# Performance work log

Hardware: AMD Instinct MI355X
Metric: run time of the kernel (lower is better)

The kernel has to match this reference:

```python
import jax, jax.numpy as jnp
import numpy as np

DIM = 512
NUM_HEADS = 16
WS = 8  # window_size
N = WS * WS
B = 1024


def get_relative_index(h, w):
    coords_h = np.arange(h)[:, None].repeat(w, axis=1)
    coords_w = np.arange(w)[None, :].repeat(h, axis=0)
    coords = np.stack([coords_h, coords_w], axis=-1).reshape(-1, 2)  # [N,2]
    rel = coords[:, None, :] - coords[None, :, :]
    rel = rel + np.array([h - 1, w - 1])
    rel[:, :, 0] *= 2 * w - 1
    return rel.sum(-1).astype(np.int32)  # [N,N]


def setup_inputs() -> dict:
    key = jax.random.key(0)
    ks = jax.random.split(key, 6)
    table_size = (2 * WS - 1) * (2 * WS - 1)  # 225
    return {
        "x": jax.random.normal(ks[0], (B, N, DIM), dtype=jnp.float32),
        "qkv_weight": jax.random.normal(ks[1], (3 * DIM, DIM), dtype=jnp.float32) * 0.02,
        "qkv_bias": jax.random.normal(ks[2], (3 * DIM,), dtype=jnp.float32) * 0.02,
        "proj_weight": jax.random.normal(ks[3], (DIM, DIM), dtype=jnp.float32) * 0.02,
        "proj_bias": jax.random.normal(ks[4], (DIM,), dtype=jnp.float32) * 0.02,
        "relative_table": jax.random.normal(ks[5], (table_size, 2 * NUM_HEADS), dtype=jnp.float32) * 0.02,
        "relative_index": jnp.asarray(get_relative_index(WS, WS)),
    }


def reference(x, qkv_weight, qkv_bias, proj_weight, proj_bias, relative_table, relative_index):
    B_, n, C = x.shape
    H = NUM_HEADS
    hd = C // H
    scale = hd ** -0.5
    # qkv projection: [B,N,3C] -> [3,B,H,N,hd]
    qkv = (x @ qkv_weight.T + qkv_bias).reshape(B_, n, 3, H, hd).transpose(2, 0, 3, 1, 4)
    q, k, v = qkv[0], qkv[1], qkv[2]
    attn = jnp.einsum("bhnd,bhmd->bhnm", q * scale, k)  # [B,H,N,N]
    # learned relative-position bias + post-softmax scale
    params = relative_table[relative_index.reshape(-1)].reshape(n, n, 2 * H)
    params = params.transpose(2, 0, 1)  # [2H,N,N]
    rel_bias, rel_scale = params[:H], params[H:]
    attn = jax.nn.softmax(attn + rel_bias[None], axis=-1)
    attn = attn * rel_scale[None]
    out = jnp.einsum("bhnm,bhmd->bhnd", attn, v)
    out = out.transpose(0, 2, 1, 3).reshape(B_, n, C)
    return out @ proj_weight.T + proj_bias
```

## Files before the change

### kernel.cpp

```cpp
#include <hip/hip_runtime.h>

typedef unsigned short u16;
typedef unsigned int   u32;
typedef __attribute__((ext_vector_type(8))) short bf16x8;
typedef __attribute__((ext_vector_type(4))) float f32x4;

#define SCALE 0.17677669529663687f

__device__ __forceinline__ u16 f2bf(float f){
  u32 x = __float_as_uint(f);
  x += 0x7fffu + ((x >> 16) & 1u);
  return (u16)(x >> 16);
}
__device__ __forceinline__ float bf2f(u16 u){
  return __uint_as_float(((u32)u) << 16);
}


__global__ void prep_kernel(const float* __restrict__ qkvw, const float* __restrict__ projw,
                            const float* __restrict__ table, const int* __restrict__ relidx,
                            u16* __restrict__ qkvw_b, u16* __restrict__ projw_b,
                            u16* __restrict__ biasT, u16* __restrict__ scaleT){
  int i = blockIdx.x * 256 + threadIdx.x;
  if (i < 786432) {
    qkvw_b[i] = f2bf(qkvw[i]);
  } else if (i < 1048576) {
    int j = i - 786432; projw_b[j] = f2bf(projw[j]);
  } else if (i < 1114112) {
    int j = i - 1048576; int h = j >> 12, rc = j & 4095;
    int idx = relidx[rc];
    int row = rc >> 6, col = rc & 63;
    int noff = h*4096 + row*64 + (col & 15)*4 + (col >> 4);
    biasT [noff] = f2bf(table[idx*32 + h]);
    scaleT[noff] = f2bf(table[idx*32 + 16 + h]);
  }
}

__global__ void xconv_kernel(const float* __restrict__ x, u16* __restrict__ xb){
  size_t i = (size_t)blockIdx.x * 256 + threadIdx.x;
  const float4* xp = (const float4*)x;
  float4 a = xp[2*i], b = xp[2*i+1];
  union { u16 u[8]; uint4 v; } o;
  o.u[0]=f2bf(a.x); o.u[1]=f2bf(a.y); o.u[2]=f2bf(a.z); o.u[3]=f2bf(a.w);
  o.u[4]=f2bf(b.x); o.u[5]=f2bf(b.y); o.u[6]=f2bf(b.z); o.u[7]=f2bf(b.w);
  *(uint4*)(xb + 8*i) = o.v;
}

template<int EPI>
__global__ __launch_bounds__(512, 2) void gemm_kernel(
    const u16* __restrict__ A, const u16* __restrict__ W,
    const float* __restrict__ bias, void* __restrict__ outp, const int NT)
{
  __shared__ u16 lds[3][16384];
  const int tid = threadIdx.x, lane = tid & 63, wid = tid >> 6;
  const int wave_base = tid & ~63;

  const int cpx = gridDim.x >> 3;
  const int bid = (blockIdx.x & 7) * cpx + (blockIdx.x >> 3);
  const int mt = bid / NT, nt = bid % NT;
  const size_t m0 = (size_t)mt * 256;
  const int n0 = nt * 256;
  const int wm = wid >> 2, wn = wid & 3;

  const f32x4 z = {0.f, 0.f, 0.f, 0.f};
  f32x4 acc[8][4];
#pragma unroll
  for (int i = 0; i < 8; i++)
#pragma unroll
    for (int j = 0; j < 4; j++) acc[i][j] = z;

  auto stageA = [&](int ch){
    const int slot = ch % 3;
    const int kb = ch * 32;
#pragma unroll
    for (int c = 0; c < 2; ++c){
      const int t = c*512 + tid;
      const int row = t >> 2, sl = t & 3;
      const int lsl = sl ^ ((row >> 1) & 3);
      const u16* ga = A + (m0 + row)*512 + kb + lsl*8;
      u16* la = &lds[slot][(size_t)(c*512 + wave_base)*8];
      __builtin_amdgcn_global_load_lds((const __attribute__((address_space(1))) u32*)ga,
                                       (__attribute__((address_space(3))) u32*)la, 16, 0, 0);
    }
  };
  auto stageB = [&](int ch){
    const int slot = ch % 3;
    const int kb = ch * 32;
#pragma unroll
    for (int c = 0; c < 2; ++c){
      const int t = c*512 + tid;
      const int col = t >> 2, sl = t & 3;
      const int lsl = sl ^ ((col >> 1) & 3);
      const u16* gb = W + (size_t)(n0 + col)*512 + kb + lsl*8;
      u16* lb = &lds[slot][8192 + (size_t)(c*512 + wave_base)*8];
      __builtin_amdgcn_global_load_lds((const __attribute__((address_space(1))) u32*)gb,
                                       (__attribute__((address_space(3))) u32*)lb, 16, 0, 0);
    }
  };

  stageA(0); stageB(0);
  stageA(1); stageB(1);
  asm volatile("s_waitcnt vmcnt(4)" ::: "memory");
  __builtin_amdgcn_s_barrier();

  const int lq = lane & 15, lk = lane >> 4;
#pragma unroll
  for (int ch = 0; ch < 16; ++ch){
    const int slot = ch % 3;
    const u16* As = &lds[slot][0];
    const u16* Bs = &lds[slot][8192];
    bf16x8 af[4], bfr[4], af2[4];

#pragma unroll
    for (int i = 0; i < 4; ++i){
      const int row = wm*128 + i*16 + lq;
      af[i]  = *(const bf16x8*)&As[row*32 + (lk ^ ((row >> 1) & 3))*8];
      const int col = wn*64 + i*16 + lq;
      bfr[i] = *(const bf16x8*)&Bs[col*32 + (lk ^ ((col >> 1) & 3))*8];
    }
    if (ch + 2 < 16) stageA(ch + 2);
    __builtin_amdgcn_s_barrier();
    asm volatile("s_waitcnt lgkmcnt(0)" ::: "memory");
    __builtin_amdgcn_sched_barrier(0);
    __builtin_amdgcn_s_setprio(1);
#pragma unroll
    for (int i = 0; i < 4; ++i)
#pragma unroll
      for (int j = 0; j < 4; ++j)
        acc[i][j] = __builtin_amdgcn_mfma_f32_16x16x32_bf16(af[i], bfr[j], acc[i][j], 0, 0, 0);
    __builtin_amdgcn_s_setprio(0);
    __builtin_amdgcn_s_barrier();

#pragma unroll
    for (int i = 0; i < 4; ++i){
      const int row = wm*128 + 64 + i*16 + lq;
      af2[i] = *(const bf16x8*)&As[row*32 + (lk ^ ((row >> 1) & 3))*8];
    }
    if (ch + 2 < 16) stageB(ch + 2);
    __builtin_amdgcn_s_barrier();
    asm volatile("s_waitcnt lgkmcnt(0)" ::: "memory");
    __builtin_amdgcn_sched_barrier(0);
    __builtin_amdgcn_s_setprio(1);
#pragma unroll
    for (int i = 0; i < 4; ++i)
#pragma unroll
      for (int j = 0; j < 4; ++j)
        acc[4+i][j] = __builtin_amdgcn_mfma_f32_16x16x32_bf16(af2[i], bfr[j], acc[4+i][j], 0, 0, 0);
    __builtin_amdgcn_s_setprio(0);
    if (ch < 14)       { asm volatile("s_waitcnt vmcnt(4)" ::: "memory"); }
    else if (ch == 14) { asm volatile("s_waitcnt vmcnt(0)" ::: "memory"); }
    if (ch < 15) __builtin_amdgcn_s_barrier();
  }

  const int lr = (lane >> 4) << 2;
  const int lc = lane & 15;
  if (EPI == 0){
    u16* o = (u16*)outp;
    float bv[4], sc[4];
#pragma unroll
    for (int nf = 0; nf < 4; ++nf){
      const int col = n0 + wn*64 + nf*16 + lc;
      bv[nf] = bias[col];
      sc[nf] = (col < 512) ? SCALE : 1.f;
    }
#pragma unroll
    for (int mf = 0; mf < 8; ++mf){
#pragma unroll
      for (int r = 0; r < 4; ++r){
        const size_t row = m0 + wm*128 + mf*16 + lr + r;
#pragma unroll
        for (int nf = 0; nf < 4; ++nf){
          const int col = n0 + wn*64 + nf*16 + lc;
          o[row*1536 + col] = f2bf((acc[mf][nf][r] + bv[nf]) * sc[nf]);
        }
      }
    }
  } else {
    float* o = (float*)outp;
    float bv[4];
#pragma unroll
    for (int nf = 0; nf < 4; ++nf)
      bv[nf] = bias[n0 + wn*64 + nf*16 + lc];
#pragma unroll
    for (int mf = 0; mf < 8; ++mf){
#pragma unroll
      for (int r = 0; r < 4; ++r){
        const size_t row = m0 + wm*128 + mf*16 + lr + r;
#pragma unroll
        for (int nf = 0; nf < 4; ++nf){
          const int col = n0 + wn*64 + nf*16 + lc;
          o[row*512 + col] = acc[mf][nf][r] + bv[nf];
        }
      }
    }
  }
}

__global__ __launch_bounds__(256) void attn_kernel(
    const u16* __restrict__ qkv, const u16* __restrict__ biasT,
    const u16* __restrict__ scaleT, u16* __restrict__ attn_out)
{
  __shared__ u16 qs[2][2560];
  __shared__ u16 ks[2][2560];
  __shared__ u16 vs[2][2560];
  __shared__ u16 Ps[4608];
  const int tid = threadIdx.x, lane = tid & 63, wid = tid >> 6;
  const int lq = lane & 15, lg = lane >> 4;
  const int row = tid >> 2, sg = (tid & 3) * 8;
  const int b  = blockIdx.x >> 3;
  const int h0 = (blockIdx.x & 7) * 2;
  const u16* pbase = qkv + ((size_t)b*64 + row)*1536 + sg;
  const int wr0 = wid * 16;
  const f32x4 z = {0.f, 0.f, 0.f, 0.f};

  auto compute = [&](int buf, int h){
    bf16x8 qf = *(const bf16x8*)&qs[buf][(wr0 + lq)*40 + lg*8];
    f32x4 s[4];
#pragma unroll
    for (int ct = 0; ct < 4; ++ct){
      bf16x8 kf = *(const bf16x8*)&ks[buf][(ct*16 + lq)*40 + lg*8];
      s[ct] = __builtin_amdgcn_mfma_f32_16x16x32_bf16(qf, kf, z, 0, 0, 0);
    }
    const u16* bT = biasT + h*4096;
    const u16* sT = scaleT + h*4096;
#pragma unroll
    for (int r = 0; r < 4; ++r){
      const int rq = wr0 + lg*4 + r;
      const ushort4 b4 = *(const ushort4*)&bT[rq*64 + lq*4];
      const ushort4 s4 = *(const ushort4*)&sT[rq*64 + lq*4];
      float vals[4];
      vals[0] = s[0][r] + bf2f(b4.x);
      vals[1] = s[1][r] + bf2f(b4.y);
      vals[2] = s[2][r] + bf2f(b4.z);
      vals[3] = s[3][r] + bf2f(b4.w);
      float mx = fmaxf(fmaxf(vals[0], vals[1]), fmaxf(vals[2], vals[3]));
      mx = fmaxf(mx, __shfl_xor(mx, 1));
      mx = fmaxf(mx, __shfl_xor(mx, 2));
      mx = fmaxf(mx, __shfl_xor(mx, 4));
      mx = fmaxf(mx, __shfl_xor(mx, 8));
      float sm = 0.f;
#pragma unroll
      for (int j = 0; j < 4; ++j){ vals[j] = __expf(vals[j] - mx); sm += vals[j]; }
      sm += __shfl_xor(sm, 1);
      sm += __shfl_xor(sm, 2);
      sm += __shfl_xor(sm, 4);
      sm += __shfl_xor(sm, 8);
      const float inv = 1.f / sm;
      const u16 sv[4] = {s4.x, s4.y, s4.z, s4.w};
#pragma unroll
      for (int j = 0; j < 4; ++j)
        Ps[rq*72 + j*16 + lq] = f2bf(vals[j] * inv * bf2f(sv[j]));
    }
    asm volatile("s_waitcnt lgkmcnt(0)" ::: "memory");
    __builtin_amdgcn_sched_barrier(0);

    f32x4 o[2] = {z, z};
#pragma unroll
    for (int kc = 0; kc < 2; ++kc){
      bf16x8 pa = *(const bf16x8*)&Ps[(wr0 + lq)*72 + kc*32 + lg*8];
#pragma unroll
      for (int c2 = 0; c2 < 2; ++c2){
        union { u16 u[8]; bf16x8 v; } vf;
#pragma unroll
        for (int e = 0; e < 8; ++e)
          vf.u[e] = vs[buf][(kc*32 + lg*8 + e)*40 + c2*16 + lq];
        o[c2] = __builtin_amdgcn_mfma_f32_16x16x32_bf16(pa, vf.v, o[c2], 0, 0, 0);
      }
    }
#pragma unroll
    for (int c2 = 0; c2 < 2; ++c2){
#pragma unroll
      for (int r = 0; r < 4; ++r){
        const int n = wr0 + lg*4 + r;
        attn_out[((size_t)b*64 + n)*512 + h*32 + c2*16 + lq] = f2bf(o[c2][r]);
      }
    }
  };

  uint4 q0 = *(const uint4*)(pbase + h0*32);
  uint4 k0 = *(const uint4*)(pbase + 512 + h0*32);
  uint4 v0 = *(const uint4*)(pbase + 1024 + h0*32);
  *(uint4*)&qs[0][row*40 + sg] = q0;
  *(uint4*)&ks[0][row*40 + sg] = k0;
  *(uint4*)&vs[0][row*40 + sg] = v0;
  uint4 q1 = *(const uint4*)(pbase + (h0+1)*32);
  uint4 k1 = *(const uint4*)(pbase + 512 + (h0+1)*32);
  uint4 v1 = *(const uint4*)(pbase + 1024 + (h0+1)*32);
  __syncthreads();

  compute(0, h0);

  *(uint4*)&qs[1][row*40 + sg] = q1;
  *(uint4*)&ks[1][row*40 + sg] = k1;
  *(uint4*)&vs[1][row*40 + sg] = v1;
  __syncthreads();

  compute(1, h0 + 1);
}

extern "C" void kernel_launch(void* const* d_in, const int* in_sizes, int n_in,
                              void* d_out, int out_size, void* d_ws, size_t ws_size,
                              hipStream_t stream)
{
  const float* x      = (const float*)d_in[0];
  const float* qkvw   = (const float*)d_in[1];
  const float* qkvb   = (const float*)d_in[2];
  const float* projw  = (const float*)d_in[3];
  const float* projb  = (const float*)d_in[4];
  const float* table  = (const float*)d_in[5];
  const int*   relidx = (const int*)d_in[6];
  char* ws = (char*)d_ws;

  u16* qkvw_b = (u16*)(ws + 0);
  u16* projw_b= (u16*)(ws + 1572864);
  u16* biasT  = (u16*)(ws + 2097152);
  u16* scaleT = (u16*)(ws + 2228224);
  u16* qkvws  = (u16*)(ws + 2359296);
  u16* xb     = (u16*)(ws + 203685888);
  u16* attn_o = xb;

  if (ws_size < 270794752ull) return;

  prep_kernel<<<dim3(4352), dim3(256), 0, stream>>>(qkvw, projw, table, relidx,
                                                    qkvw_b, projw_b, biasT, scaleT);
  xconv_kernel<<<dim3(16384), dim3(256), 0, stream>>>(x, xb);
  gemm_kernel<0><<<dim3(1536), dim3(512), 0, stream>>>(xb, qkvw_b, qkvb, (void*)qkvws, 6);
  attn_kernel<<<dim3(8192), dim3(256), 0, stream>>>(qkvws, biasT, scaleT, attn_o);
  gemm_kernel<1><<<dim3(512), dim3(512), 0, stream>>>(attn_o, projw_b, projb, d_out, 2);
}
```

Before: 284.1 us.

## Write QKV GEMM output in per-head layout with transposed V, swizzle attention LDS

The QKV GEMM epilogue now scatters Q and K into contiguous per-batch, per-head [64x32] tiles and writes V transposed ([d][token]) into a separate buffer. The attention kernel can then load each head's tiles contiguously and read V fragments with single 128-bit LDS loads, replacing eight scalar loads. Padded LDS strides are replaced by XOR swizzles to avoid bank conflicts. The cost is a more scattered, uncoalesced store pattern in the GEMM epilogue, especially for the transposed V writes.

Measured after the change: 328.5 us. 1.16x slower.

```diff
diff --git a/kernel.cpp b/kernel.cpp
--- a/kernel.cpp
+++ b/kernel.cpp
@@ -155,23 +155,40 @@
   const int lr = (lane >> 4) << 2;
   const int lc = lane & 15;
   if (EPI == 0){
-    u16* o = (u16*)outp;
-    float bv[4], sc[4];
+    u16* o  = (u16*)outp;
+    u16* ov = o + 67108864;
+    const int which = n0 >> 9;
+    float bv[4], sc; int pb[4];
+    sc = (which == 0) ? SCALE : 1.f;
 #pragma unroll
     for (int nf = 0; nf < 4; ++nf){
       const int col = n0 + wn*64 + nf*16 + lc;
       bv[nf] = bias[col];
-      sc[nf] = (col < 512) ? SCALE : 1.f;
-    }
-#pragma unroll
-    for (int mf = 0; mf < 8; ++mf){
-#pragma unroll
-      for (int r = 0; r < 4; ++r){
-        const size_t row = m0 + wm*128 + mf*16 + lr + r;
-#pragma unroll
-        for (int nf = 0; nf < 4; ++nf){
-          const int col = n0 + wn*64 + nf*16 + lc;
-          o[row*1536 + col] = f2bf((acc[mf][nf][r] + bv[nf]) * sc[nf]);
+      const int h = (col >> 5) & 15, d = col & 31;
+      pb[nf] = (which < 2) ? ((h*2 + which)*2048 + d) : (h*2048 + d*64);
+    }
+    if (which < 2){
+#pragma unroll
+      for (int mf = 0; mf < 8; ++mf){
+#pragma unroll
+        for (int r = 0; r < 4; ++r){
+          const int row = (int)m0 + wm*128 + mf*16 + lr + r;
+          const size_t base = (size_t)(row >> 6) * 65536 + (row & 63)*32;
+#pragma unroll
+          for (int nf = 0; nf < 4; ++nf)
+            o[base + pb[nf]] = f2bf((acc[mf][nf][r] + bv[nf]) * sc);
+        }
+      }
+    } else {
+#pragma unroll
+      for (int mf = 0; mf < 8; ++mf){
+#pragma unroll
+        for (int r = 0; r < 4; ++r){
+          const int row = (int)m0 + wm*128 + mf*16 + lr + r;
+          const size_t base = (size_t)(row >> 6) * 32768 + (row & 63);
+#pragma unroll
+          for (int nf = 0; nf < 4; ++nf)
+            ov[base + pb[nf]] = f2bf(acc[mf][nf][r] + bv[nf]);
         }
       }
     }
@@ -197,28 +214,33 @@
 }
 
 __global__ __launch_bounds__(256) void attn_kernel(
-    const u16* __restrict__ qkv, const u16* __restrict__ biasT,
-    const u16* __restrict__ scaleT, u16* __restrict__ attn_out)
+    const u16* __restrict__ qk, const u16* __restrict__ vT,
+    const u16* __restrict__ biasT, const u16* __restrict__ scaleT,
+    u16* __restrict__ attn_out)
 {
-  __shared__ u16 qs[2][2560];
-  __shared__ u16 ks[2][2560];
-  __shared__ u16 vs[2][2560];
-  __shared__ u16 Ps[4608];
+  __shared__ u16 qs[2][2048];
+  __shared__ u16 ks[2][2048];
+  __shared__ u16 vts[2][2048];
+  __shared__ u16 Ps[4096];
   const int tid = threadIdx.x, lane = tid & 63, wid = tid >> 6;
   const int lq = lane & 15, lg = lane >> 4;
-  const int row = tid >> 2, sg = (tid & 3) * 8;
+  const int row = tid >> 2, sl = tid & 3;
+  const int vd = tid >> 3, vsl = tid & 7;
   const int b  = blockIdx.x >> 3;
   const int h0 = (blockIdx.x & 7) * 2;
-  const u16* pbase = qkv + ((size_t)b*64 + row)*1536 + sg;
+  const u16* qkb = qk + (size_t)b * 65536;
+  const u16* vb  = vT + (size_t)b * 32768;
   const int wr0 = wid * 16;
   const f32x4 z = {0.f, 0.f, 0.f, 0.f};
 
   auto compute = [&](int buf, int h){
-    bf16x8 qf = *(const bf16x8*)&qs[buf][(wr0 + lq)*40 + lg*8];
+    const int qrow = wr0 + lq;
+    bf16x8 qf = *(const bf16x8*)&qs[buf][qrow*32 + (lg ^ ((qrow >> 1) & 3))*8];
     f32x4 s[4];
 #pragma unroll
     for (int ct = 0; ct < 4; ++ct){
-      bf16x8 kf = *(const bf16x8*)&ks[buf][(ct*16 + lq)*40 + lg*8];
+      const int krow = ct*16 + lq;
+      bf16x8 kf = *(const bf16x8*)&ks[buf][krow*32 + (lg ^ ((krow >> 1) & 3))*8];
       s[ct] = __builtin_amdgcn_mfma_f32_16x16x32_bf16(qf, kf, z, 0, 0, 0);
     }
     const u16* bT = biasT + h*4096;
@@ -248,8 +270,10 @@
       const float inv = 1.f / sm;
       const u16 sv[4] = {s4.x, s4.y, s4.z, s4.w};
 #pragma unroll
-      for (int j = 0; j < 4; ++j)
-        Ps[rq*72 + j*16 + lq] = f2bf(vals[j] * inv * bf2f(sv[j]));
+      for (int j = 0; j < 4; ++j){
+        const int cs = j*2 + (lq >> 3);
+        Ps[rq*64 + (cs ^ (rq & 7))*8 + (lq & 7)] = f2bf(vals[j] * inv * bf2f(sv[j]));
+      }
     }
     asm volatile("s_waitcnt lgkmcnt(0)" ::: "memory");
     __builtin_amdgcn_sched_barrier(0);
@@ -257,14 +281,13 @@
     f32x4 o[2] = {z, z};
 #pragma unroll
     for (int kc = 0; kc < 2; ++kc){
-      bf16x8 pa = *(const bf16x8*)&Ps[(wr0 + lq)*72 + kc*32 + lg*8];
+      const int prow = wr0 + lq;
+      bf16x8 pa = *(const bf16x8*)&Ps[prow*64 + ((kc*4 + lg) ^ (prow & 7))*8];
 #pragma unroll
       for (int c2 = 0; c2 < 2; ++c2){
-        union { u16 u[8]; bf16x8 v; } vf;
-#pragma unroll
-        for (int e = 0; e < 8; ++e)
-          vf.u[e] = vs[buf][(kc*32 + lg*8 + e)*40 + c2*16 + lq];
-        o[c2] = __builtin_amdgcn_mfma_f32_16x16x32_bf16(pa, vf.v, o[c2], 0, 0, 0);
+        const int d = c2*16 + lq;
+        bf16x8 vf = *(const bf16x8*)&vts[buf][d*64 + ((kc*4 + lg) ^ (d & 7))*8];
+        o[c2] = __builtin_amdgcn_mfma_f32_16x16x32_bf16(pa, vf, o[c2], 0, 0, 0);
       }
     }
 #pragma unroll
@@ -277,22 +300,22 @@
     }
   };
 
-  uint4 q0 = *(const uint4*)(pbase + h0*32);
-  uint4 k0 = *(const uint4*)(pbase + 512 + h0*32);
-  uint4 v0 = *(const uint4*)(pbase + 1024 + h0*32);
-  *(uint4*)&qs[0][row*40 + sg] = q0;
-  *(uint4*)&ks[0][row*40 + sg] = k0;
-  *(uint4*)&vs[0][row*40 + sg] = v0;
-  uint4 q1 = *(const uint4*)(pbase + (h0+1)*32);
-  uint4 k1 = *(const uint4*)(pbase + 512 + (h0+1)*32);
-  uint4 v1 = *(const uint4*)(pbase + 1024 + (h0+1)*32);
+  uint4 q0 = *(const uint4*)(qkb + h0*4096 + row*32 + sl*8);
+  uint4 k0 = *(const uint4*)(qkb + h0*4096 + 2048 + row*32 + sl*8);
+  uint4 v0 = *(const uint4*)(vb + h0*2048 + vd*64 + vsl*8);
+  *(uint4*)&qs[0][row*32 + (sl ^ ((row >> 1) & 3))*8] = q0;
+  *(uint4*)&ks[0][row*32 + (sl ^ ((row >> 1) & 3))*8] = k0;
+  *(uint4*)&vts[0][vd*64 + (vsl ^ (vd & 7))*8] = v0;
+  uint4 q1 = *(const uint4*)(qkb + (h0+1)*4096 + row*32 + sl*8);
+  uint4 k1 = *(const uint4*)(qkb + (h0+1)*4096 + 2048 + row*32 + sl*8);
+  uint4 v1 = *(const uint4*)(vb + (h0+1)*2048 + vd*64 + vsl*8);
   __syncthreads();
 
   compute(0, h0);
 
-  *(uint4*)&qs[1][row*40 + sg] = q1;
-  *(uint4*)&ks[1][row*40 + sg] = k1;
-  *(uint4*)&vs[1][row*40 + sg] = v1;
+  *(uint4*)&qs[1][row*32 + (sl ^ ((row >> 1) & 3))*8] = q1;
+  *(uint4*)&ks[1][row*32 + (sl ^ ((row >> 1) & 3))*8] = k1;
+  *(uint4*)&vts[1][vd*64 + (vsl ^ (vd & 7))*8] = v1;
   __syncthreads();
 
   compute(1, h0 + 1);
@@ -315,7 +338,8 @@
   u16* projw_b= (u16*)(ws + 1572864);
   u16* biasT  = (u16*)(ws + 2097152);
   u16* scaleT = (u16*)(ws + 2228224);
-  u16* qkvws  = (u16*)(ws + 2359296);
+  u16* qkbuf  = (u16*)(ws + 2359296);
+  u16* vTbuf  = (u16*)(ws + 136577024);
   u16* xb     = (u16*)(ws + 203685888);
   u16* attn_o = xb;
 
@@ -324,7 +348,7 @@
   prep_kernel<<<dim3(4352), dim3(256), 0, stream>>>(qkvw, projw, table, relidx,
                                                     qkvw_b, projw_b, biasT, scaleT);
   xconv_kernel<<<dim3(16384), dim3(256), 0, stream>>>(x, xb);
-  gemm_kernel<0><<<dim3(1536), dim3(512), 0, stream>>>(xb, qkvw_b, qkvb, (void*)qkvws, 6);
-  attn_kernel<<<dim3(8192), dim3(256), 0, stream>>>(qkvws, biasT, scaleT, attn_o);
+  gemm_kernel<0><<<dim3(1536), dim3(512), 0, stream>>>(xb, qkvw_b, qkvb, (void*)qkbuf, 6);
+  attn_kernel<<<dim3(8192), dim3(256), 0, stream>>>(qkbuf, vTbuf, biasT, scaleT, attn_o);
   gemm_kernel<1><<<dim3(512), dim3(512), 0, stream>>>(attn_o, projw_b, projb, d_out, 2);
 }
```

## Fuse fp32-to-bf16 conversion of x into the QKV GEMM loader

Applied to the files above, without the earlier changes.

Removes the separate x conversion kernel and has the QKV GEMM stream fp32 x directly into LDS, converting to bf16 in registers with packed cvt instructions before the MFMAs. This drops one full write and re-read of a bf16 copy of x plus a launch. In exchange the QKV GEMM loads twice as many bytes for A per tile (fp32), uses a larger LDS footprint (3x48KB), and adds conversion ALU work inside the main loop, which could hurt occupancy since each block (launch bounds 512, 2) now needs 144 KB of LDS. The GEMM template is split into two specialised kernels.

After: 310.0 us. 9.1% more time.

```diff
diff --git a/kernel.cpp b/kernel.cpp
--- a/kernel.cpp
+++ b/kernel.cpp
@@ -14,6 +14,14 @@
 }
 __device__ __forceinline__ float bf2f(u16 u){
   return __uint_as_float(((u32)u) << 16);
+}
+__device__ __forceinline__ bf16x8 cvt8(f32x4 a, f32x4 b){
+  union { u32 w[4]; bf16x8 v; } r;
+  asm("v_cvt_pk_bf16_f32 %0, %1, %2" : "=v"(r.w[0]) : "v"(a[0]), "v"(a[1]));
+  asm("v_cvt_pk_bf16_f32 %0, %1, %2" : "=v"(r.w[1]) : "v"(a[2]), "v"(a[3]));
+  asm("v_cvt_pk_bf16_f32 %0, %1, %2" : "=v"(r.w[2]) : "v"(b[0]), "v"(b[1]));
+  asm("v_cvt_pk_bf16_f32 %0, %1, %2" : "=v"(r.w[3]) : "v"(b[2]), "v"(b[3]));
+  return r.v;
 }
 
 
@@ -36,20 +44,141 @@
   }
 }
 
-__global__ void xconv_kernel(const float* __restrict__ x, u16* __restrict__ xb){
-  size_t i = (size_t)blockIdx.x * 256 + threadIdx.x;
-  const float4* xp = (const float4*)x;
-  float4 a = xp[2*i], b = xp[2*i+1];
-  union { u16 u[8]; uint4 v; } o;
-  o.u[0]=f2bf(a.x); o.u[1]=f2bf(a.y); o.u[2]=f2bf(a.z); o.u[3]=f2bf(a.w);
-  o.u[4]=f2bf(b.x); o.u[5]=f2bf(b.y); o.u[6]=f2bf(b.z); o.u[7]=f2bf(b.w);
-  *(uint4*)(xb + 8*i) = o.v;
-}
-
-template<int EPI>
-__global__ __launch_bounds__(512, 2) void gemm_kernel(
+__global__ __launch_bounds__(512, 2) void gemm_qkv_kernel(
+    const float* __restrict__ X, const u16* __restrict__ W,
+    const float* __restrict__ bias, u16* __restrict__ outp)
+{
+  __shared__ u16 lds[3][24576];
+  const int tid = threadIdx.x, lane = tid & 63, wid = tid >> 6;
+  const int wave_base = tid & ~63;
+
+  const int cpx = gridDim.x >> 3;
+  const int bid = (blockIdx.x & 7) * cpx + (blockIdx.x >> 3);
+  const int mt = bid / 6, nt = bid % 6;
+  const size_t m0 = (size_t)mt * 256;
+  const int n0 = nt * 256;
+  const int wm = wid >> 2, wn = wid & 3;
+
+  const f32x4 z = {0.f, 0.f, 0.f, 0.f};
+  f32x4 acc[8][4];
+#pragma unroll
+  for (int i = 0; i < 8; i++)
+#pragma unroll
+    for (int j = 0; j < 4; j++) acc[i][j] = z;
+
+  auto stageA = [&](int ch){
+    const int slot = ch % 3;
+    const int kb = ch * 32;
+#pragma unroll
+    for (int c = 0; c < 4; ++c){
+      const int t = c*512 + tid;
+      const int row = t >> 3, sl = t & 7;
+      const float* ga = X + (m0 + row)*512 + kb + ((sl ^ (row & 7)) << 2);
+      u16* la = &lds[slot][(size_t)(c*512 + wave_base)*8];
+      __builtin_amdgcn_global_load_lds((const __attribute__((address_space(1))) u32*)ga,
+                                       (__attribute__((address_space(3))) u32*)la, 16, 0, 0);
+    }
+  };
+  auto stageB = [&](int ch){
+    const int slot = ch % 3;
+    const int kb = ch * 32;
+#pragma unroll
+    for (int c = 0; c < 2; ++c){
+      const int t = c*512 + tid;
+      const int col = t >> 2, sl = t & 3;
+      const int lsl = sl ^ ((col >> 1) & 3);
+      const u16* gb = W + (size_t)(n0 + col)*512 + kb + lsl*8;
+      u16* lb = &lds[slot][16384 + (size_t)(c*512 + wave_base)*8];
+      __builtin_amdgcn_global_load_lds((const __attribute__((address_space(1))) u32*)gb,
+                                       (__attribute__((address_space(3))) u32*)lb, 16, 0, 0);
+    }
+  };
+
+  stageA(0); stageB(0);
+  stageA(1); stageB(1);
+  asm volatile("s_waitcnt vmcnt(6)" ::: "memory");
+  __builtin_amdgcn_s_barrier();
+
+  const int lq = lane & 15, lk = lane >> 4;
+#pragma unroll
+  for (int ch = 0; ch < 16; ++ch){
+    const int slot = ch % 3;
+    const float* Af = (const float*)&lds[slot][0];
+    const u16*   Bs = &lds[slot][16384];
+    bf16x8 af[4], bfr[4], af2[4];
+
+#pragma unroll
+    for (int i = 0; i < 4; ++i){
+      const int row = wm*128 + i*16 + lq;
+      f32x4 a0 = *(const f32x4*)&Af[row*32 + ((lk*2    ) ^ (row & 7))*4];
+      f32x4 a1 = *(const f32x4*)&Af[row*32 + ((lk*2 + 1) ^ (row & 7))*4];
+      af[i] = cvt8(a0, a1);
+      const int col = wn*64 + i*16 + lq;
+      bfr[i] = *(const bf16x8*)&Bs[col*32 + (lk ^ ((col >> 1) & 3))*8];
+    }
+    if (ch + 2 < 16) stageA(ch + 2);
+    __builtin_amdgcn_s_barrier();
+    asm volatile("s_waitcnt lgkmcnt(0)" ::: "memory");
+    __builtin_amdgcn_sched_barrier(0);
+    __builtin_amdgcn_s_setprio(1);
+#pragma unroll
+    for (int i = 0; i < 4; ++i)
+#pragma unroll
+      for (int j = 0; j < 4; ++j)
+        acc[i][j] = __builtin_amdgcn_mfma_f32_16x16x32_bf16(af[i], bfr[j], acc[i][j], 0, 0, 0);
+    __builtin_amdgcn_s_setprio(0);
+    __builtin_amdgcn_s_barrier();
+
+#pragma unroll
+    for (int i = 0; i < 4; ++i){
+      const int row = wm*128 + 64 + i*16 + lq;
+      f32x4 a0 = *(const f32x4*)&Af[row*32 + ((lk*2    ) ^ (row & 7))*4];
+      f32x4 a1 = *(const f32x4*)&Af[row*32 + ((lk*2 + 1) ^ (row & 7))*4];
+      af2[i] = cvt8(a0, a1);
+    }
+    if (ch + 2 < 16) stageB(ch + 2);
+    __builtin_amdgcn_s_barrier();
+    asm volatile("s_waitcnt lgkmcnt(0)" ::: "memory");
+    __builtin_amdgcn_sched_barrier(0);
+    __builtin_amdgcn_s_setprio(1);
+#pragma unroll
+    for (int i = 0; i < 4; ++i)
+#pragma unroll
+      for (int j = 0; j < 4; ++j)
+        acc[4+i][j] = __builtin_amdgcn_mfma_f32_16x16x32_bf16(af2[i], bfr[j], acc[4+i][j], 0, 0, 0);
+    __builtin_amdgcn_s_setprio(0);
+    if (ch < 14)       { asm volatile("s_waitcnt vmcnt(6)" ::: "memory"); }
+    else if (ch == 14) { asm volatile("s_waitcnt vmcnt(0)" ::: "memory"); }
+    if (ch < 15) __builtin_amdgcn_s_barrier();
+  }
+
+  const int lr = (lane >> 4) << 2;
+  const int lc = lane & 15;
+  u16* o = outp;
+  float bv[4], sc[4];
+#pragma unroll
+  for (int nf = 0; nf < 4; ++nf){
+    const int col = n0 + wn*64 + nf*16 + lc;
+    bv[nf] = bias[col];
+    sc[nf] = (col < 512) ? SCALE : 1.f;
+  }
+#pragma unroll
+  for (int mf = 0; mf < 8; ++mf){
+#pragma unroll
+    for (int r = 0; r < 4; ++r){
+      const size_t row = m0 + wm*128 + mf*16 + lr + r;
+#pragma unroll
+      for (int nf = 0; nf < 4; ++nf){
+        const int col = n0 + wn*64 + nf*16 + lc;
+        o[row*1536 + col] = f2bf((acc[mf][nf][r] + bv[nf]) * sc[nf]);
+      }
+    }
+  }
+}
+
+__global__ __launch_bounds__(512, 2) void gemm_proj_kernel(
     const u16* __restrict__ A, const u16* __restrict__ W,
-    const float* __restrict__ bias, void* __restrict__ outp, const int NT)
+    const float* __restrict__ bias, float* __restrict__ outp)
 {
   __shared__ u16 lds[3][16384];
   const int tid = threadIdx.x, lane = tid & 63, wid = tid >> 6;
@@ -57,7 +186,7 @@
 
   const int cpx = gridDim.x >> 3;
   const int bid = (blockIdx.x & 7) * cpx + (blockIdx.x >> 3);
-  const int mt = bid / NT, nt = bid % NT;
+  const int mt = bid >> 1, nt = bid & 1;
   const size_t m0 = (size_t)mt * 256;
   const int n0 = nt * 256;
   const int wm = wid >> 2, wn = wid & 3;
@@ -154,43 +283,19 @@
 
   const int lr = (lane >> 4) << 2;
   const int lc = lane & 15;
-  if (EPI == 0){
-    u16* o = (u16*)outp;
-    float bv[4], sc[4];
-#pragma unroll
-    for (int nf = 0; nf < 4; ++nf){
-      const int col = n0 + wn*64 + nf*16 + lc;
-      bv[nf] = bias[col];
-      sc[nf] = (col < 512) ? SCALE : 1.f;
-    }
-#pragma unroll
-    for (int mf = 0; mf < 8; ++mf){
-#pragma unroll
-      for (int r = 0; r < 4; ++r){
-        const size_t row = m0 + wm*128 + mf*16 + lr + r;
-#pragma unroll
-        for (int nf = 0; nf < 4; ++nf){
-          const int col = n0 + wn*64 + nf*16 + lc;
-          o[row*1536 + col] = f2bf((acc[mf][nf][r] + bv[nf]) * sc[nf]);
-        }
-      }
-    }
-  } else {
-    float* o = (float*)outp;
-    float bv[4];
-#pragma unroll
-    for (int nf = 0; nf < 4; ++nf)
-      bv[nf] = bias[n0 + wn*64 + nf*16 + lc];
-#pragma unroll
-    for (int mf = 0; mf < 8; ++mf){
-#pragma unroll
-      for (int r = 0; r < 4; ++r){
-        const size_t row = m0 + wm*128 + mf*16 + lr + r;
-#pragma unroll
-        for (int nf = 0; nf < 4; ++nf){
-          const int col = n0 + wn*64 + nf*16 + lc;
-          o[row*512 + col] = acc[mf][nf][r] + bv[nf];
-        }
+  float bv[4];
+#pragma unroll
+  for (int nf = 0; nf < 4; ++nf)
+    bv[nf] = bias[n0 + wn*64 + nf*16 + lc];
+#pragma unroll
+  for (int mf = 0; mf < 8; ++mf){
+#pragma unroll
+    for (int r = 0; r < 4; ++r){
+      const size_t row = m0 + wm*128 + mf*16 + lr + r;
+#pragma unroll
+      for (int nf = 0; nf < 4; ++nf){
+        const int col = n0 + wn*64 + nf*16 + lc;
+        outp[row*512 + col] = acc[mf][nf][r] + bv[nf];
       }
     }
   }
@@ -316,15 +421,13 @@
   u16* biasT  = (u16*)(ws + 2097152);
   u16* scaleT = (u16*)(ws + 2228224);
   u16* qkvws  = (u16*)(ws + 2359296);
-  u16* xb     = (u16*)(ws + 203685888);
-  u16* attn_o = xb;
+  u16* attn_o = (u16*)(ws + 203685888);
 
   if (ws_size < 270794752ull) return;
 
   prep_kernel<<<dim3(4352), dim3(256), 0, stream>>>(qkvw, projw, table, relidx,
                                                     qkvw_b, projw_b, biasT, scaleT);
-  xconv_kernel<<<dim3(16384), dim3(256), 0, stream>>>(x, xb);
-  gemm_kernel<0><<<dim3(1536), dim3(512), 0, stream>>>(xb, qkvw_b, qkvb, (void*)qkvws, 6);
+  gemm_qkv_kernel<<<dim3(1536), dim3(512), 0, stream>>>(x, qkvw_b, qkvb, qkvws);
   attn_kernel<<<dim3(8192), dim3(256), 0, stream>>>(qkvws, biasT, scaleT, attn_o);
-  gemm_kernel<1><<<dim3(512), dim3(512), 0, stream>>>(attn_o, projw_b, projb, d_out, 2);
-}
+  gemm_proj_kernel<<<dim3(512), dim3(512), 0, stream>>>(attn_o, projw_b, projb, (float*)d_out);
+}
```
